# Optimization experiments

Hardware: AMD Instinct MI355X
Metric: run time of the kernel (lower is better)

## Reference

```python
import jax, jax.numpy as jnp
import numpy as np

H = 16  # num_heads


def setup_inputs() -> dict:
    key = jax.random.key(0)
    ks = jax.random.split(key, 8)
    B, N, C = 16, 4096, 512
    hd = C // H
    sc = lambda k, shape: jax.random.normal(k, shape, jnp.float32) * 0.02
    return {
        "x": jax.random.normal(ks[0], (B, N, C), jnp.float32),
        "Wqkv": sc(ks[1], (C, 3 * C)),
        "bqkv": sc(ks[2], (3 * C,)),
        "pos_enc": jnp.zeros((1, N, C), jnp.float32),
        "dwc_w": sc(ks[3], (hd, 1, 5, 5)),  # OIHW, depthwise: groups = hd
        "dwc_b": sc(ks[4], (hd,)),
        "Wproj": sc(ks[5], (C, C)),
        "bproj": sc(ks[6], (C,)),
    }


def reference(x, Wqkv, bqkv, pos_enc, dwc_w, dwc_b, Wproj, bproj):
    B, N, C = x.shape
    hd = C // H
    # qkv projection
    qkv = x @ Wqkv + bqkv                       # (B, N, 3C)
    q, k, v = jnp.split(qkv, 3, axis=-1)
    k = k + pos_enc
    q = jax.nn.relu(q)
    k = jax.nn.relu(k)

    def heads(t):  # (B, N, C) -> (B*H, N, hd), fp32 as in the torch autocast-off block
        return t.reshape(B, N, H, hd).transpose(0, 2, 1, 3).reshape(B * H, N, hd).astype(jnp.float32)

    q, k, v = heads(q), heads(k), heads(v)
    # normalization z_i = 1 / (q_i . sum_j k_j + eps)
    z = 1.0 / (jnp.einsum('bic,bc->bi', q, k.sum(axis=1)) + 1e-6)   # (B*H, N)
    # kv-first path: i*j*(c+d) > c*d*(i+j) for N=4096, hd=32
    kv = jnp.einsum('bjc,bjd->bcd', k, v)                           # (B*H, hd, hd)
    out = jnp.einsum('bic,bcd->bid', q, kv) * z[..., None]          # (B*H, N, hd)
    # depthwise 5x5 conv on v reshaped to a square feature map
    w = int(N ** 0.5)
    fm = v.transpose(0, 2, 1).reshape(B * H, hd, w, w)
    fm = jax.lax.conv_general_dilated(
        fm, dwc_w, window_strides=(1, 1), padding=[(2, 2), (2, 2)],
        dimension_numbers=('NCHW', 'OIHW', 'NCHW'), feature_group_count=hd)
    fm = fm + dwc_b[None, :, None, None]
    fm = fm.reshape(B * H, hd, N).transpose(0, 2, 1)
    out = out + fm
    # merge heads and project
    out = out.reshape(B, H, N, hd).transpose(0, 2, 1, 3).reshape(B, N, C)
    return out @ Wproj + bproj
```

## Files before the change

### kernel.cpp

```cpp
#include <hip/hip_runtime.h>
#include <stdint.h>

typedef short bf16x8 __attribute__((ext_vector_type(8)));
typedef float f32x4 __attribute__((ext_vector_type(4)));
typedef unsigned short u16x8 __attribute__((ext_vector_type(8)));

__device__ __forceinline__ unsigned short f2bf(float f){
  uint32_t u = __builtin_bit_cast(uint32_t, f);
  u += 0x7FFFu + ((u >> 16) & 1u);
  return (unsigned short)(u >> 16);
}
__device__ __forceinline__ float bf2f(unsigned short h){
  uint32_t u = ((uint32_t)h) << 16;
  return __builtin_bit_cast(float, u);
}
__device__ __forceinline__ float bflo(uint32_t dw){
  return __builtin_bit_cast(float, dw << 16);
}
__device__ __forceinline__ float bfhi(uint32_t dw){
  return __builtin_bit_cast(float, dw & 0xffff0000u);
}

__device__ __forceinline__ void gload_lds16(const void* g, void* l){
  __builtin_amdgcn_global_load_lds(
      (const __attribute__((address_space(1))) uint32_t*)(g),
      (__attribute__((address_space(3))) uint32_t*)(l),
      16, 0, 0);
}

__global__ __launch_bounds__(256) void convert_x_k(const float* __restrict__ x,
                                                   unsigned short* __restrict__ xb){
  size_t i = (size_t)blockIdx.x * 256 + threadIdx.x;
  const float4* p = (const float4*)x + i * 2;
  float4 a = p[0], b = p[1];
  u16x8 o;
  o[0] = f2bf(a.x); o[1] = f2bf(a.y); o[2] = f2bf(a.z); o[3] = f2bf(a.w);
  o[4] = f2bf(b.x); o[5] = f2bf(b.y); o[6] = f2bf(b.z); o[7] = f2bf(b.w);
  *(u16x8*)(xb + i * 8) = o;
}

__global__ __launch_bounds__(256) void transpose_w_k(const float* __restrict__ Wqkv,
                                                     const float* __restrict__ Wproj,
                                                     unsigned short* __restrict__ Wqkvt,
                                                     unsigned short* __restrict__ Wprojt){
  __shared__ unsigned short t[64][68];
  int bid = blockIdx.x;
  const float* src; unsigned short* dst; int c0, j0, sstride, dstride;
  if (bid < 192){
    src = Wqkv;  dst = Wqkvt;  sstride = 1536; dstride = 512;
    c0 = (bid / 24) * 64;  j0 = (bid % 24) * 64;
  } else {
    int e = bid - 192;
    src = Wproj; dst = Wprojt; sstride = 512;  dstride = 512;
    c0 = (e >> 3) * 64;    j0 = (e & 7) * 64;
  }
  int tid = threadIdx.x;
  int rl = tid >> 6;
  int cl = tid & 63;
  #pragma unroll
  for (int i = 0; i < 16; ++i){
    int cr = i * 4 + rl;
    t[cl][cr] = f2bf(src[(size_t)(c0 + cr) * sstride + j0 + cl]);
  }
  __syncthreads();
  #pragma unroll
  for (int i = 0; i < 16; ++i){
    int jr = i * 4 + rl;
    dst[(size_t)(j0 + jr) * dstride + c0 + cl] = t[jr][cl];
  }
}

template<int EPI>
__device__ __forceinline__ void gemm_body(
    const unsigned short* __restrict__ A,
    const unsigned short* __restrict__ Bt,
    const float* __restrict__ bias,
    const float* __restrict__ pos_enc,
    unsigned short* __restrict__ oq,
    unsigned short* __restrict__ ok,
    unsigned short* __restrict__ ov,
    float* __restrict__ op,
    int NTN)
{
  __shared__ unsigned short As[256 * 64];
  __shared__ unsigned short Bs[128 * 64];
  int tid = threadIdx.x, lane = tid & 63, wid = tid >> 6;
  int nwg = gridDim.x;
  int b0 = blockIdx.x;
  int cpx = nwg >> 3;
  int swz = (b0 & 7) * cpx + (b0 >> 3);
  int tm = swz / NTN, tn = swz - tm * NTN;
  int row0 = tm << 8, col0 = tn << 7;
  int wr = wid >> 1, wc = wid & 1;

  f32x4 acc[4][4];
  #pragma unroll
  for (int m = 0; m < 4; ++m)
    #pragma unroll
    for (int n = 0; n < 4; ++n)
      acc[m][n] = (f32x4){0.f, 0.f, 0.f, 0.f};

  for (int kt = 0; kt < 8; ++kt){
    int k0 = kt * 64;
    #pragma unroll
    for (int it = 0; it < 4; ++it){
      int c = it * 512 + tid;
      int r = c >> 3;
      int scs = ((c & 7) ^ (r & 7)) * 8;
      gload_lds16(A + (size_t)(row0 + r) * 512 + k0 + scs, &As[c * 8]);
    }
    #pragma unroll
    for (int it = 0; it < 2; ++it){
      int c = it * 512 + tid;
      int r = c >> 3;
      int scs = ((c & 7) ^ (r & 7)) * 8;
      gload_lds16(Bt + (size_t)(col0 + r) * 512 + k0 + scs, &Bs[c * 8]);
    }
    __syncthreads();
    #pragma unroll
    for (int kk = 0; kk < 2; ++kk){
      bf16x8 af[4], bfr[4];
      int kcs = ((kk * 4 + (lane >> 4)) ^ (lane & 7)) * 8;
      #pragma unroll
      for (int m = 0; m < 4; ++m)
        af[m] = *(const bf16x8*)&As[(wr * 64 + m * 16 + (lane & 15)) * 64 + kcs];
      #pragma unroll
      for (int n = 0; n < 4; ++n)
        bfr[n] = *(const bf16x8*)&Bs[(wc * 64 + n * 16 + (lane & 15)) * 64 + kcs];
      #pragma unroll
      for (int m = 0; m < 4; ++m)
        #pragma unroll
        for (int n = 0; n < 4; ++n)
          acc[m][n] = __builtin_amdgcn_mfma_f32_16x16x32_bf16(af[m], bfr[n], acc[m][n], 0, 0, 0);
    }
    __syncthreads();
  }

  if constexpr (EPI == 0){
    int part = col0 >> 9;
    int ccb = (col0 & 511) + wc * 64;
    unsigned short* scr = &As[wid * 2048];
    #pragma unroll
    for (int mh = 0; mh < 2; ++mh){
      #pragma unroll
      for (int mm = 0; mm < 2; ++mm){
        int m = mh * 2 + mm;
        #pragma unroll
        for (int n = 0; n < 4; ++n){
          #pragma unroll
          for (int r = 0; r < 4; ++r){
            int lrow = mm * 16 + (lane >> 4) * 4 + r;
            int lcol = n * 16 + (lane & 15);
            float val = acc[m][n][r] + bias[col0 + wc * 64 + lcol];
            if (part == 0) val = fmaxf(val, 0.f);
            int pch = (lcol >> 3) ^ ((lrow >> 2) & 3);
            scr[lrow * 64 + pch * 8 + (lcol & 7)] = f2bf(val);
          }
        }
      }
      #pragma unroll
      for (int i = 0; i < 4; ++i){
        int idx = i * 64 + lane;
        int r2 = idx >> 3, c2 = idx & 7;
        int pch = c2 ^ ((r2 >> 2) & 3);
        u16x8 vals = *(const u16x8*)&scr[r2 * 64 + pch * 8];
        int grow = row0 + wr * 64 + mh * 32 + r2;
        int bb = grow >> 12, nn = grow & 4095;
        int cc = ccb + c2 * 8;
        int h = cc >> 5, d = cc & 31;
        size_t dst = ((size_t)((bb << 4) + h) * 4096 + nn) * 32 + d;
        if (part == 1){
          const float4* pe = (const float4*)(pos_enc + (size_t)nn * 512 + cc);
          float4 p0 = pe[0], p1 = pe[1];
          u16x8 o;
          o[0] = f2bf(fmaxf(bf2f(vals[0]) + p0.x, 0.f));
          o[1] = f2bf(fmaxf(bf2f(vals[1]) + p0.y, 0.f));
          o[2] = f2bf(fmaxf(bf2f(vals[2]) + p0.z, 0.f));
          o[3] = f2bf(fmaxf(bf2f(vals[3]) + p0.w, 0.f));
          o[4] = f2bf(fmaxf(bf2f(vals[4]) + p1.x, 0.f));
          o[5] = f2bf(fmaxf(bf2f(vals[5]) + p1.y, 0.f));
          o[6] = f2bf(fmaxf(bf2f(vals[6]) + p1.z, 0.f));
          o[7] = f2bf(fmaxf(bf2f(vals[7]) + p1.w, 0.f));
          *(u16x8*)(ok + dst) = o;
        } else if (part == 0){
          *(u16x8*)(oq + dst) = vals;
        } else {
          *(u16x8*)(ov + dst) = vals;
        }
      }
    }
  } else {
    #pragma unroll
    for (int m = 0; m < 4; ++m){
      #pragma unroll
      for (int n = 0; n < 4; ++n){
        #pragma unroll
        for (int r = 0; r < 4; ++r){
          int rrow = row0 + wr * 64 + m * 16 + (lane >> 4) * 4 + r;
          int ccol = col0 + wc * 64 + n * 16 + (lane & 15);
          op[(size_t)rrow * 512 + ccol] = acc[m][n][r] + bias[ccol];
        }
      }
    }
  }
}

__global__ __launch_bounds__(512, 2) void gemm_qkv(
    const unsigned short* __restrict__ A, const unsigned short* __restrict__ Bt,
    const float* __restrict__ bias, const float* __restrict__ pos_enc,
    unsigned short* __restrict__ oq, unsigned short* __restrict__ ok,
    unsigned short* __restrict__ ov, int NTN){
  gemm_body<0>(A, Bt, bias, pos_enc, oq, ok, ov, nullptr, NTN);
}

__global__ __launch_bounds__(512, 2) void gemm_proj(
    const unsigned short* __restrict__ A, const unsigned short* __restrict__ Bt,
    const float* __restrict__ bias, float* __restrict__ op, int NTN){
  gemm_body<1>(A, Bt, bias, nullptr, nullptr, nullptr, nullptr, op, NTN);
}

__global__ __launch_bounds__(256) void transpose_v_k(
    const unsigned short* __restrict__ vbuf, uint32_t* __restrict__ vp){
  __shared__ uint32_t tile[256][17];
  int chunk = blockIdx.x & 15;
  int bh    = blockIdx.x >> 4;
  int tid = threadIdx.x;
  const unsigned short* src = vbuf + (size_t)bh * 131072 + (size_t)chunk * 256 * 32;
  #pragma unroll
  for (int i = 0; i < 4; ++i){
    u16x8 vv = *(const u16x8*)(src + tid * 32 + i * 8);
    uint4 q = __builtin_bit_cast(uint4, vv);
    tile[tid][i * 4 + 0] = q.x;
    tile[tid][i * 4 + 1] = q.y;
    tile[tid][i * 4 + 2] = q.z;
    tile[tid][i * 4 + 3] = q.w;
  }
  __syncthreads();
  uint32_t* dstb = vp + (size_t)bh * 65536 + chunk * 256;
  #pragma unroll
  for (int i = 0; i < 16; ++i){
    dstb[i * 4096 + tid] = tile[tid][i];
  }
}

__global__ __launch_bounds__(256, 2) void attn_k3(
    const unsigned short* __restrict__ qbuf,
    const uint32_t* __restrict__ vp,
    const float* __restrict__ kvb,
    const float* __restrict__ ksb,
    const float* __restrict__ dwc_w,
    const float* __restrict__ dwc_b,
    unsigned short* __restrict__ attn)
{
  int band = blockIdx.x;
  int bh   = blockIdx.y;
  int tid = threadIdx.x, lane = tid & 63, w = tid >> 6;
  __shared__ uint32_t outs32[1024][18];
  unsigned short* outs = (unsigned short*)outs32;
  __shared__ float zs[1024];
  __shared__ float ksum_s[32];

  const unsigned short* qb = qbuf + (size_t)bh * 4096 * 32 + (size_t)band * 1024 * 32;
  const uint32_t* vpb = vp + (size_t)bh * 65536;

  if (tid < 32) ksum_s[tid] = ksb[bh * 32 + tid];
  __syncthreads();

  for (int p = 0; p < 4; ++p){
    int t = p * 256 + tid;
    float zd = 0.f;
    #pragma unroll
    for (int pp = 0; pp < 4; ++pp){
      u16x8 qq = *(const u16x8*)(qb + (size_t)t * 32 + pp * 8);
      #pragma unroll
      for (int i = 0; i < 8; ++i) zd += bf2f(qq[i]) * ksum_s[pp * 8 + i];
    }
    zs[t] = 1.f / (zd + 1e-6f);
  }

  bf16x8 bfr[2];
  #pragma unroll
  for (int nc = 0; nc < 2; ++nc){
    bf16x8 t8;
    #pragma unroll
    for (int j = 0; j < 8; ++j){
      int c = (lane >> 4) * 8 + j;
      int d = nc * 16 + (lane & 15);
      t8[j] = (short)f2bf(kvb[bh * 1024 + c * 32 + d]);
    }
    bfr[nc] = t8;
  }
  __syncthreads();

  for (int p = 0; p < 4; ++p){
    f32x4 acc[4][2];
    #pragma unroll
    for (int m = 0; m < 4; ++m){ acc[m][0] = (f32x4){0.f,0.f,0.f,0.f}; acc[m][1] = (f32x4){0.f,0.f,0.f,0.f}; }
    #pragma unroll
    for (int m = 0; m < 4; ++m){
      int row = p * 256 + w * 64 + m * 16 + (lane & 15);
      bf16x8 af = *(const bf16x8*)(qb + (size_t)row * 32 + (lane >> 4) * 8);
      acc[m][0] = __builtin_amdgcn_mfma_f32_16x16x32_bf16(af, bfr[0], acc[m][0], 0, 0, 0);
      acc[m][1] = __builtin_amdgcn_mfma_f32_16x16x32_bf16(af, bfr[1], acc[m][1], 0, 0, 0);
    }
    #pragma unroll
    for (int m = 0; m < 4; ++m)
      #pragma unroll
      for (int nc = 0; nc < 2; ++nc)
        #pragma unroll
        for (int r = 0; r < 4; ++r){
          int lrow = p * 256 + w * 64 + m * 16 + (lane >> 4) * 4 + r;
          int col = nc * 16 + (lane & 15);
          outs[lrow * 36 + col] = f2bf(acc[m][nc][r] * zs[lrow]);
        }
  }
  __syncthreads();

  int x = lane;
  int y0 = band * 16;
  int xm2 = lane - 2, xm1 = lane - 1, xp1 = lane + 1, xp2 = lane + 2;

  for (int pair = 0; pair < 4; ++pair){
    int dbase = w * 8 + pair * 2;
    int pr = w * 4 + pair;
    float w0[25], w1[25];
    #pragma unroll
    for (int j = 0; j < 25; ++j){
      w0[j] = dwc_w[dbase * 25 + j];
      w1[j] = dwc_w[(dbase + 1) * 25 + j];
    }
    float cb0 = dwc_b[dbase], cb1 = dwc_b[dbase + 1];

    uint32_t rowd[20];
    #pragma unroll
    for (int il = 0; il < 20; ++il){
      int yi = y0 - 2 + il;
      rowd[il] = (yi >= 0 && yi < 64)
        ? vpb[pr * 4096 + yi * 64 + x] : 0u;
    }

    float a0[5], a1[5];
    #pragma unroll
    for (int il = 0; il < 20; ++il){
      uint32_t d0 = rowd[il];
      uint32_t dm2 = (uint32_t)__shfl((int)d0, xm2); if (lane < 2)  dm2 = 0;
      uint32_t dm1 = (uint32_t)__shfl((int)d0, xm1); if (lane < 1)  dm1 = 0;
      uint32_t dp1 = (uint32_t)__shfl((int)d0, xp1); if (lane > 62) dp1 = 0;
      uint32_t dp2 = (uint32_t)__shfl((int)d0, xp2); if (lane > 61) dp2 = 0;
      float f0[5], f1[5];
      f0[0] = bflo(dm2); f1[0] = bfhi(dm2);
      f0[1] = bflo(dm1); f1[1] = bfhi(dm1);
      f0[2] = bflo(d0);  f1[2] = bfhi(d0);
      f0[3] = bflo(dp1); f1[3] = bfhi(dp1);
      f0[4] = bflo(dp2); f1[4] = bfhi(dp2);
      #pragma unroll
      for (int ky = 0; ky < 5; ++ky){
        int ol = il - ky;
        if (ol < 0 || ol > 15) continue;
        int s = ol % 5;
        if (ky == 0){
          a0[s] = w0[0] * f0[0];
          a1[s] = w1[0] * f1[0];
          #pragma unroll
          for (int kx = 1; kx < 5; ++kx){
            a0[s] += w0[kx] * f0[kx];
            a1[s] += w1[kx] * f1[kx];
          }
        } else {
          #pragma unroll
          for (int kx = 0; kx < 5; ++kx){
            a0[s] += w0[ky * 5 + kx] * f0[kx];
            a1[s] += w1[ky * 5 + kx] * f1[kx];
          }
        }
      }
      if (il >= 4){
        int ol = il - 4;
        int s = ol % 5;
        int ltok = ol * 64 + x;
        uint32_t ov = outs32[ltok][pr];
        float o0 = bflo(ov) + a0[s] + cb0;
        float o1 = bfhi(ov) + a1[s] + cb1;
        outs32[ltok][pr] = ((uint32_t)f2bf(o1) << 16) | (uint32_t)f2bf(o0);
      }
    }
  }
  __syncthreads();

  int b = bh >> 4, h = bh & 15;
  size_t gbase = ((size_t)b * 4096 + (size_t)band * 1024) * 512 + h * 32;
  #pragma unroll
  for (int it = 0; it < 32; ++it){
    int idx = it * 256 + tid;
    int token = idx >> 3, sub = idx & 7;
    uint2 vv = *(const uint2*)&outs32[token][sub * 2];
    *(uint2*)(attn + gbase + (size_t)token * 512 + sub * 4) = vv;
  }
}

__global__ __launch_bounds__(256) void kv_k(const unsigned short* __restrict__ kbuf,
                                            const unsigned short* __restrict__ vbuf,
                                            float* __restrict__ kvb,
                                            float* __restrict__ ksb){
  int bh  = blockIdx.x >> 2;
  int seg = blockIdx.x & 3;
  __shared__ float ks[64][36];
  __shared__ float vs[64][36];
  __shared__ float red[4][64][16];
  __shared__ float ksred[4][8][4];
  int tid = threadIdx.x;
  int g = tid >> 6, gi = tid & 63;
  int c0 = (gi >> 3) * 4, d0 = (gi & 7) * 4;
  float acc[4][4] = {};
  float ksacc[4] = {0.f, 0.f, 0.f, 0.f};
  const unsigned short* kb = kbuf + (size_t)bh * 4096 * 32 + (size_t)seg * 1024 * 32;
  const unsigned short* vb = vbuf + (size_t)bh * 4096 * 32 + (size_t)seg * 1024 * 32;
  int er = tid >> 2;
  int ec = (tid & 3) * 8;
  for (int t = 0; t < 16; ++t){
    __syncthreads();
    u16x8 kk8 = *(const u16x8*)(kb + ((size_t)t * 64 + er) * 32 + ec);
    u16x8 vv8 = *(const u16x8*)(vb + ((size_t)t * 64 + er) * 32 + ec);
    #pragma unroll
    for (int i = 0; i < 8; ++i){ ks[er][ec + i] = bf2f(kk8[i]); vs[er][ec + i] = bf2f(vv8[i]); }
    __syncthreads();
    for (int nn = g; nn < 64; nn += 4){
      f32x4 k4 = *(const f32x4*)&ks[nn][c0];
      f32x4 v4 = *(const f32x4*)&vs[nn][d0];
      #pragma unroll
      for (int i = 0; i < 4; ++i)
        #pragma unroll
        for (int j = 0; j < 4; ++j)
          acc[i][j] += k4[i] * v4[j];
      if ((gi & 7) == 0){
        #pragma unroll
        for (int i = 0; i < 4; ++i) ksacc[i] += k4[i];
      }
    }
  }
  __syncthreads();
  #pragma unroll
  for (int i = 0; i < 4; ++i)
    #pragma unroll
    for (int j = 0; j < 4; ++j)
      red[g][gi][i * 4 + j] = acc[i][j];
  if ((gi & 7) == 0){
    #pragma unroll
    for (int i = 0; i < 4; ++i) ksred[g][gi >> 3][i] = ksacc[i];
  }
  __syncthreads();
  for (int s = tid; s < 1024; s += 256){
    int gi2 = s >> 4, e = s & 15;
    float sum = red[0][gi2][e] + red[1][gi2][e] + red[2][gi2][e] + red[3][gi2][e];
    int c = (gi2 >> 3) * 4 + (e >> 2), d = (gi2 & 7) * 4 + (e & 3);
    atomicAdd(&kvb[bh * 1024 + c * 32 + d], sum);
  }
  if (tid < 32){
    float s = ksred[0][tid >> 2][tid & 3] + ksred[1][tid >> 2][tid & 3]
            + ksred[2][tid >> 2][tid & 3] + ksred[3][tid >> 2][tid & 3];
    atomicAdd(&ksb[bh * 32 + tid], s);
  }
}

extern "C" void kernel_launch(void* const* d_in, const int* in_sizes, int n_in,
                              void* d_out, int out_size, void* d_ws, size_t ws_size,
                              hipStream_t stream) {
  const float* x       = (const float*)d_in[0];
  const float* Wqkv    = (const float*)d_in[1];
  const float* bqkv    = (const float*)d_in[2];
  const float* pos_enc = (const float*)d_in[3];
  const float* dwc_w   = (const float*)d_in[4];
  const float* dwc_b   = (const float*)d_in[5];
  const float* Wproj   = (const float*)d_in[6];
  const float* bproj   = (const float*)d_in[7];
  float* out = (float*)d_out;
  char* ws = (char*)d_ws;

  const size_t off_xb    = 0;
  const size_t off_wqkvt = 67108864;
  const size_t off_wprojt= 68681728;
  const size_t off_q     = 69206016;
  const size_t off_k     = 136314880;
  const size_t off_v     = 203423744;
  const size_t off_kv    = 270532608;
  const size_t off_ksum  = 271581184;
  const size_t needed    = 271613952;
  if (ws_size < needed) return;

  unsigned short* xb     = (unsigned short*)(ws + off_xb);
  unsigned short* wqkvt  = (unsigned short*)(ws + off_wqkvt);
  unsigned short* wprojt = (unsigned short*)(ws + off_wprojt);
  unsigned short* qb     = (unsigned short*)(ws + off_q);
  unsigned short* kb     = (unsigned short*)(ws + off_k);
  unsigned short* vb     = (unsigned short*)(ws + off_v);
  float* kvb = (float*)(ws + off_kv);
  float* ksb = (float*)(ws + off_ksum);
  unsigned short* attn = kb;
  uint32_t* vp = (uint32_t*)(ws + off_xb);

  convert_x_k<<<16384, 256, 0, stream>>>(x, xb);
  transpose_w_k<<<256, 256, 0, stream>>>(Wqkv, Wproj, wqkvt, wprojt);
  gemm_qkv<<<3072, 512, 0, stream>>>(xb, wqkvt, bqkv, pos_enc, qb, kb, vb, 12);
  (void)hipMemsetAsync(kvb, 0, (size_t)(256 * 1024 + 256 * 32) * sizeof(float), stream);
  transpose_v_k<<<4096, 256, 0, stream>>>(vb, vp);
  kv_k<<<1024, 256, 0, stream>>>(kb, vb, kvb, ksb);
  attn_k3<<<dim3(4, 256), 256, 0, stream>>>(qb, vp, kvb, ksb, dwc_w, dwc_b, attn);
  gemm_proj<<<1024, 512, 0, stream>>>(attn, wprojt, bproj, out, 4);
}
```

Before: 420.2 us.

## Double-buffer GEMM LDS tiles and widen block tile to 256x256

The shared GEMM body is restructured to use 256x256 output tiles with 8x4 MFMA accumulators per wave. Global-to-LDS loads are double-buffered with explicit vmcnt waits so the next K tile loads while the current one computes, and MFMA sections run at raised wave priority. Grid sizes for the QKV and projection GEMMs are halved to match. The larger tile and doubled LDS (128KB) lower occupancy to one block per CU and raise register pressure, trading latency hiding across blocks for more reuse and overlap within a block.

```diff
diff --git a/kernel.cpp b/kernel.cpp
--- a/kernel.cpp
+++ b/kernel.cpp
@@ -82,66 +82,85 @@
     float* __restrict__ op,
     int NTN)
 {
-  __shared__ unsigned short As[256 * 64];
-  __shared__ unsigned short Bs[128 * 64];
+  __shared__ unsigned short As[2][256 * 64];
+  __shared__ unsigned short Bs[2][256 * 64];
   int tid = threadIdx.x, lane = tid & 63, wid = tid >> 6;
   int nwg = gridDim.x;
   int b0 = blockIdx.x;
   int cpx = nwg >> 3;
   int swz = (b0 & 7) * cpx + (b0 >> 3);
   int tm = swz / NTN, tn = swz - tm * NTN;
-  int row0 = tm << 8, col0 = tn << 7;
-  int wr = wid >> 1, wc = wid & 1;
-
-  f32x4 acc[4][4];
-  #pragma unroll
-  for (int m = 0; m < 4; ++m)
+  int row0 = tm << 8, col0 = tn << 8;
+  int wrow = wid >> 2, wcol = wid & 3;
+
+  f32x4 acc[8][4];
+  #pragma unroll
+  for (int m = 0; m < 8; ++m)
     #pragma unroll
     for (int n = 0; n < 4; ++n)
       acc[m][n] = (f32x4){0.f, 0.f, 0.f, 0.f};
 
-  for (int kt = 0; kt < 8; ++kt){
+  auto STAGE = [&](int buf, int kt){
     int k0 = kt * 64;
     #pragma unroll
     for (int it = 0; it < 4; ++it){
       int c = it * 512 + tid;
       int r = c >> 3;
       int scs = ((c & 7) ^ (r & 7)) * 8;
-      gload_lds16(A + (size_t)(row0 + r) * 512 + k0 + scs, &As[c * 8]);
-    }
-    #pragma unroll
-    for (int it = 0; it < 2; ++it){
+      gload_lds16(A + (size_t)(row0 + r) * 512 + k0 + scs, &As[buf][c * 8]);
+    }
+    #pragma unroll
+    for (int it = 0; it < 4; ++it){
       int c = it * 512 + tid;
       int r = c >> 3;
       int scs = ((c & 7) ^ (r & 7)) * 8;
-      gload_lds16(Bt + (size_t)(col0 + r) * 512 + k0 + scs, &Bs[c * 8]);
-    }
-    __syncthreads();
+      gload_lds16(Bt + (size_t)(col0 + r) * 512 + k0 + scs, &Bs[buf][c * 8]);
+    }
+  };
+  auto COMPUTE = [&](int buf){
+    bf16x8 bfr[4][2];
     #pragma unroll
     for (int kk = 0; kk < 2; ++kk){
-      bf16x8 af[4], bfr[4];
       int kcs = ((kk * 4 + (lane >> 4)) ^ (lane & 7)) * 8;
       #pragma unroll
-      for (int m = 0; m < 4; ++m)
-        af[m] = *(const bf16x8*)&As[(wr * 64 + m * 16 + (lane & 15)) * 64 + kcs];
-      #pragma unroll
       for (int n = 0; n < 4; ++n)
-        bfr[n] = *(const bf16x8*)&Bs[(wc * 64 + n * 16 + (lane & 15)) * 64 + kcs];
-      #pragma unroll
-      for (int m = 0; m < 4; ++m)
+        bfr[n][kk] = *(const bf16x8*)&Bs[buf][(wcol * 64 + n * 16 + (lane & 15)) * 64 + kcs];
+    }
+    __builtin_amdgcn_s_setprio(1);
+    #pragma unroll
+    for (int kk = 0; kk < 2; ++kk){
+      int kcs = ((kk * 4 + (lane >> 4)) ^ (lane & 7)) * 8;
+      #pragma unroll
+      for (int m = 0; m < 8; ++m){
+        bf16x8 af = *(const bf16x8*)&As[buf][(wrow * 128 + m * 16 + (lane & 15)) * 64 + kcs];
         #pragma unroll
         for (int n = 0; n < 4; ++n)
-          acc[m][n] = __builtin_amdgcn_mfma_f32_16x16x32_bf16(af[m], bfr[n], acc[m][n], 0, 0, 0);
-    }
-    __syncthreads();
+          acc[m][n] = __builtin_amdgcn_mfma_f32_16x16x32_bf16(af, bfr[n][kk], acc[m][n], 0, 0, 0);
+      }
+    }
+    __builtin_amdgcn_s_setprio(0);
+  };
+
+  STAGE(0, 0);
+  STAGE(1, 1);
+  #pragma unroll
+  for (int t = 0; t < 8; ++t){
+    if (t < 7) asm volatile("s_waitcnt vmcnt(8)" ::: "memory");
+    else       asm volatile("s_waitcnt vmcnt(0)" ::: "memory");
+    __builtin_amdgcn_s_barrier();
+    __builtin_amdgcn_sched_barrier(0);
+    COMPUTE(t & 1);
+    asm volatile("" ::: "memory");
+    __builtin_amdgcn_s_barrier();
+    if (t + 2 < 8) STAGE(t & 1, t + 2);
   }
 
   if constexpr (EPI == 0){
     int part = col0 >> 9;
-    int ccb = (col0 & 511) + wc * 64;
-    unsigned short* scr = &As[wid * 2048];
-    #pragma unroll
-    for (int mh = 0; mh < 2; ++mh){
+    int ccb = (col0 & 511) + wcol * 64;
+    unsigned short* scr = &As[0][wid * 2048];
+    #pragma unroll
+    for (int mh = 0; mh < 4; ++mh){
       #pragma unroll
       for (int mm = 0; mm < 2; ++mm){
         int m = mh * 2 + mm;
@@ -151,7 +170,7 @@
           for (int r = 0; r < 4; ++r){
             int lrow = mm * 16 + (lane >> 4) * 4 + r;
             int lcol = n * 16 + (lane & 15);
-            float val = acc[m][n][r] + bias[col0 + wc * 64 + lcol];
+            float val = acc[m][n][r] + bias[col0 + wcol * 64 + lcol];
             if (part == 0) val = fmaxf(val, 0.f);
             int pch = (lcol >> 3) ^ ((lrow >> 2) & 3);
             scr[lrow * 64 + pch * 8 + (lcol & 7)] = f2bf(val);
@@ -164,7 +183,7 @@
         int r2 = idx >> 3, c2 = idx & 7;
         int pch = c2 ^ ((r2 >> 2) & 3);
         u16x8 vals = *(const u16x8*)&scr[r2 * 64 + pch * 8];
-        int grow = row0 + wr * 64 + mh * 32 + r2;
+        int grow = row0 + wrow * 128 + mh * 32 + r2;
         int bb = grow >> 12, nn = grow & 4095;
         int cc = ccb + c2 * 8;
         int h = cc >> 5, d = cc & 31;
@@ -191,13 +210,13 @@
     }
   } else {
     #pragma unroll
-    for (int m = 0; m < 4; ++m){
+    for (int m = 0; m < 8; ++m){
       #pragma unroll
       for (int n = 0; n < 4; ++n){
         #pragma unroll
         for (int r = 0; r < 4; ++r){
-          int rrow = row0 + wr * 64 + m * 16 + (lane >> 4) * 4 + r;
-          int ccol = col0 + wc * 64 + n * 16 + (lane & 15);
+          int rrow = row0 + wrow * 128 + m * 16 + (lane >> 4) * 4 + r;
+          int ccol = col0 + wcol * 64 + n * 16 + (lane & 15);
           op[(size_t)rrow * 512 + ccol] = acc[m][n][r] + bias[ccol];
         }
       }
@@ -205,7 +224,7 @@
   }
 }
 
-__global__ __launch_bounds__(512, 2) void gemm_qkv(
+__global__ __launch_bounds__(512, 1) void gemm_qkv(
     const unsigned short* __restrict__ A, const unsigned short* __restrict__ Bt,
     const float* __restrict__ bias, const float* __restrict__ pos_enc,
     unsigned short* __restrict__ oq, unsigned short* __restrict__ ok,
@@ -213,7 +232,7 @@
   gemm_body<0>(A, Bt, bias, pos_enc, oq, ok, ov, nullptr, NTN);
 }
 
-__global__ __launch_bounds__(512, 2) void gemm_proj(
+__global__ __launch_bounds__(512, 1) void gemm_proj(
     const unsigned short* __restrict__ A, const unsigned short* __restrict__ Bt,
     const float* __restrict__ bias, float* __restrict__ op, int NTN){
   gemm_body<1>(A, Bt, bias, nullptr, nullptr, nullptr, nullptr, op, NTN);
@@ -500,10 +519,10 @@
 
   convert_x_k<<<16384, 256, 0, stream>>>(x, xb);
   transpose_w_k<<<256, 256, 0, stream>>>(Wqkv, Wproj, wqkvt, wprojt);
-  gemm_qkv<<<3072, 512, 0, stream>>>(xb, wqkvt, bqkv, pos_enc, qb, kb, vb, 12);
+  gemm_qkv<<<1536, 512, 0, stream>>>(xb, wqkvt, bqkv, pos_enc, qb, kb, vb, 6);
   (void)hipMemsetAsync(kvb, 0, (size_t)(256 * 1024 + 256 * 32) * sizeof(float), stream);
   transpose_v_k<<<4096, 256, 0, stream>>>(vb, vp);
   kv_k<<<1024, 256, 0, stream>>>(kb, vb, kvb, ksb);
   attn_k3<<<dim3(4, 256), 256, 0, stream>>>(qb, vp, kvb, ksb, dwc_w, dwc_b, attn);
-  gemm_proj<<<1024, 512, 0, stream>>>(attn, wprojt, bproj, out, 4);
-}
+  gemm_proj<<<512, 512, 0, stream>>>(attn, wprojt, bproj, out, 2);
+}
```

Result: faster. 400.4 us (-4.7%).
